# Kernel tuning notes

Measured on AMD Instinct MI355X. Metric: run time of the kernel, lower is better.

Reference implementation:

```python
import jax, jax.numpy as jnp
import numpy as np

B, NP, NL, CIN, COUT, MID = 2048, 8, 4, 256, 256, 64


def setup_inputs() -> dict:
    key = jax.random.key(0)
    ks = jax.random.split(key, 16)
    s = 0.01  # small init scale (code uses xavier_normal with tiny gain)
    inp = {
        "x": jax.random.normal(ks[0], (B, CIN), jnp.float32),
        "h": jax.random.normal(ks[1], (B, NP), jnp.float32),
        "index": jnp.zeros((NL,), jnp.float32).at[0].set(1.0),  # one-hot layer index
        # target Linear params
        "target_w": jax.random.normal(ks[2], (COUT, CIN), jnp.float32) * (1.0 / np.sqrt(CIN)),
        "target_b": jax.random.normal(ks[3], (COUT,), jnp.float32) * 0.01,
        # embedder weight branch
        "fcwp_w": jax.random.normal(ks[4], (MID * CIN, NP), jnp.float32) * s,
        "fcwp_b": jnp.zeros((MID * CIN,), jnp.float32),
        "fcwi_w": jax.random.normal(ks[5], (MID * CIN, NL), jnp.float32) * s,
        "fcwi_b": jnp.zeros((MID * CIN,), jnp.float32),
        "fcwe_w": jax.random.normal(ks[6], (COUT, MID), jnp.float32) * s,
        "fcwe_b": jnp.zeros((COUT,), jnp.float32),
        # embedder bias branch
        "fcbp_w": jax.random.normal(ks[7], (COUT, NP), jnp.float32) * s,
        "fcbp_b": jnp.zeros((COUT,), jnp.float32),
        "fcbi_w": jax.random.normal(ks[8], (COUT, NL), jnp.float32) * s,
        "fcbi_b": jnp.zeros((COUT,), jnp.float32),
    }
    return inp


def reference(x, h, index, target_w, target_b,
              fcwp_w, fcwp_b, fcwi_w, fcwi_b, fcwe_w, fcwe_b,
              fcbp_w, fcbp_b, fcbi_w, fcbi_b):
    # --- embedder: per-sample weight modulation ---
    # w_flat: (B, mid*cin)
    w_flat = h @ fcwp_w.T + fcwp_b + (index @ fcwi_w.T + fcwi_b)
    w = w_flat.reshape(B, CIN, MID)                      # (B, cin, mid)
    w = jnp.einsum('bim,om->boi', w, fcwe_w) + fcwe_b[None, :, None]  # swapaxes folded in -> (B, out, cin)
    # bias modulation: (B, out)
    b = h @ fcbp_w.T + fcbp_b + (index @ fcbi_w.T + fcbi_b)
    # --- per-sample linear (grouped conv2d == batched GEMM) ---
    weights = target_w[None] + w                         # (B, out, cin)
    y = jnp.einsum('bi,boi->bo', x, weights)             # batched matvec
    y = y + target_b[None, :] + b
    return y
```

## Files before the change

### kernel.cpp

```cpp
#include <hip/hip_runtime.h>


#define B_TOT 2048
#define NP    8
#define CIN   256
#define COUT  256
#define MID   64
#define NB1   576
#define K2    352
#define LDG   576
#define LDAS  136
#define LDA2S 360
#define LDB2S 360

typedef short  short8  __attribute__((ext_vector_type(8)));
typedef float  floatx4 __attribute__((ext_vector_type(4)));

__device__ __forceinline__ unsigned short f2bf(float f) {
    union { float f; unsigned u; } v; v.f = f;
    unsigned r = v.u + 0x7FFFu + ((v.u >> 16) & 1u);
    return (unsigned short)(r >> 16);
}
__device__ __forceinline__ float bf2f(unsigned short u) {
    union { unsigned u; float f; } v; v.u = ((unsigned)u) << 16;
    return v.f;
}

__global__ __launch_bounds__(256) void setup_kernel(
    const float* __restrict__ x, const float* __restrict__ h,
    const float* __restrict__ index,
    const float* __restrict__ target_w, const float* __restrict__ target_b,
    const float* __restrict__ fcwp_w, const float* __restrict__ fcwp_b,
    const float* __restrict__ fcwi_w, const float* __restrict__ fcwi_b,
    const float* __restrict__ fcwe_w, const float* __restrict__ fcwe_b,
    const float* __restrict__ fcbp_w, const float* __restrict__ fcbp_b,
    const float* __restrict__ fcbi_w, const float* __restrict__ fcbi_b,
    unsigned short* __restrict__ Bb, unsigned short* __restrict__ B2,
    unsigned short* __restrict__ A2)
{
    __shared__ unsigned short Lt[64][68];
    __shared__ float red[32][8];
    const int blk = blockIdx.x, tid = threadIdx.x;

    if (blk < 32) {
        const int i0 = (blk >> 3) * 64, n0 = (blk & 7) * 64;
        const int r = tid >> 4, c4 = (tid & 15) * 4;
        #pragma unroll
        for (int k = 0; k < 4; ++k) {
            int ii = r + k * 16;
            float4 v = *(const float4*)(fcwp_w + (size_t)(i0 + ii) * 512 + n0 + c4);
            Lt[c4 + 0][ii] = f2bf(v.x); Lt[c4 + 1][ii] = f2bf(v.y);
            Lt[c4 + 2][ii] = f2bf(v.z); Lt[c4 + 3][ii] = f2bf(v.w);
        }
        __syncthreads();
        const int nn = tid >> 2, ic0 = (tid & 3) * 16;
        #pragma unroll
        for (int k = 0; k < 4; ++k) {
            int ic = ic0 + k * 4;
            ushort4 o4;
            o4.x = Lt[nn][ic]; o4.y = Lt[nn][ic + 1];
            o4.z = Lt[nn][ic + 2]; o4.w = Lt[nn][ic + 3];
            *(ushort4*)&Bb[(size_t)(n0 + nn) * CIN + i0 + ic] = o4;
        }
    } else if (blk < 36) {
        const int i0 = (blk - 32) * 64;
        const float x0 = index[0], x1 = index[1], x2 = index[2], x3 = index[3];
        const int r = tid >> 4, c4 = (tid & 15) * 4;
        #pragma unroll
        for (int k = 0; k < 4; ++k) {
            int ii = r + k * 16;
            int e = (i0 + ii) * 64 + c4;
            float4 pb = *(const float4*)(fcwp_b + e);
            float4 ib = *(const float4*)(fcwi_b + e);
            float pbv[4] = {pb.x, pb.y, pb.z, pb.w};
            float ibv[4] = {ib.x, ib.y, ib.z, ib.w};
            #pragma unroll
            for (int j = 0; j < 4; ++j) {
                float4 wv = *(const float4*)(fcwi_w + (size_t)(e + j) * 4);
                Lt[c4 + j][ii] = f2bf(pbv[j] + ibv[j]
                    + x0 * wv.x + x1 * wv.y + x2 * wv.z + x3 * wv.w);
            }
        }
        __syncthreads();
        const int mm = tid >> 2, ic0 = (tid & 3) * 16;
        #pragma unroll
        for (int k = 0; k < 4; ++k) {
            int ic = ic0 + k * 4;
            ushort4 o4;
            o4.x = Lt[mm][ic]; o4.y = Lt[mm][ic + 1];
            o4.z = Lt[mm][ic + 2]; o4.w = Lt[mm][ic + 3];
            *(ushort4*)&Bb[(size_t)(512 + mm) * CIN + i0 + ic] = o4;
        }
    } else if (blk < 52) {
        int base = (blk - 36) * 4096;
        #pragma unroll
        for (int k = 0; k < 4; ++k) {
            int e = base + k * 1024 + tid * 4;
            int o = e >> 8, c = e & 255;
            float4 v = *(const float4*)(target_w + e);
            ushort4 o4;
            o4.x = f2bf(v.x); o4.y = f2bf(v.y); o4.z = f2bf(v.z); o4.w = f2bf(v.w);
            *(ushort4*)&B2[(size_t)o * K2 + c] = o4;
        }
    } else if (blk < 56) {
        int base = (blk - 52) * 4096;
        #pragma unroll
        for (int k = 0; k < 4; ++k) {
            int e = base + k * 1024 + tid * 4;
            int o = e >> 6, m = e & 63;
            float4 v = *(const float4*)(fcwe_w + e);
            ushort4 o4;
            o4.x = f2bf(v.x); o4.y = f2bf(v.y); o4.z = f2bf(v.z); o4.w = f2bf(v.w);
            *(ushort4*)&B2[(size_t)o * K2 + 256 + m] = o4;
        }
    } else if (blk == 56) {
        int o = tid;
        size_t bo = (size_t)o * K2;
        float4 p0 = *(const float4*)(fcbp_w + (size_t)o * 8);
        float4 p1 = *(const float4*)(fcbp_w + (size_t)o * 8 + 4);
        B2[bo + 320] = f2bf(p0.x); B2[bo + 321] = f2bf(p0.y);
        B2[bo + 322] = f2bf(p0.z); B2[bo + 323] = f2bf(p0.w);
        B2[bo + 324] = f2bf(p1.x); B2[bo + 325] = f2bf(p1.y);
        B2[bo + 326] = f2bf(p1.z); B2[bo + 327] = f2bf(p1.w);
        B2[bo + 328] = f2bf(fcwe_b[o]);
        float bc = target_b[o] + fcbp_b[o] + fcbi_b[o]
                 + index[0] * fcbi_w[o * 4]     + index[1] * fcbi_w[o * 4 + 1]
                 + index[2] * fcbi_w[o * 4 + 2] + index[3] * fcbi_w[o * 4 + 3];
        B2[bo + 329] = f2bf(bc);
        #pragma unroll
        for (int z = 330; z < K2; ++z) B2[bo + z] = 0;
    } else {
        const int r0 = (blk - 57) * 32;
        const int rr = tid >> 3, cpos = tid & 7;
        const int b = r0 + rr;
        const float* xrow = x + (size_t)b * CIN;
        float psum = 0.f;
        #pragma unroll
        for (int k = 0; k < 8; ++k) {
            int c = (cpos + k * 8) * 4;
            float4 v = *(const float4*)(xrow + c);
            psum += v.x + v.y + v.z + v.w;
            ushort4 o4;
            o4.x = f2bf(v.x); o4.y = f2bf(v.y); o4.z = f2bf(v.z); o4.w = f2bf(v.w);
            *(ushort4*)&A2[(size_t)b * K2 + c] = o4;
        }
        red[rr][cpos] = psum;
        A2[(size_t)b * K2 + 320 + cpos] = f2bf(h[(size_t)r0 * NP + tid]);
        for (int idx = tid; idx < 32 * 22; idx += 256) {
            int r2 = idx / 22, c2 = 330 + idx % 22;
            A2[(size_t)(r0 + r2) * K2 + c2] = 0;
        }
        __syncthreads();
        if (tid < 32) {
            float s = red[tid][0] + red[tid][1] + red[tid][2] + red[tid][3]
                    + red[tid][4] + red[tid][5] + red[tid][6] + red[tid][7];
            size_t base = (size_t)(r0 + tid) * K2;
            A2[base + 328] = f2bf(s);
            A2[base + 329] = 0x3F80;
        }
    }
}

__global__ __launch_bounds__(256) void gemm1_kernel(
    const unsigned short* __restrict__ A2,
    const unsigned short* __restrict__ Bb,
    unsigned short* __restrict__ G)
{
    __shared__ unsigned short As[64 * LDAS];
    __shared__ unsigned short Bs[64 * LDAS];

    const int tid = threadIdx.x, lane = tid & 63, w = tid >> 6;
    const int col = lane & 15, quad = lane >> 4;
    const int mb = blockIdx.x * 64, nb = blockIdx.y * 64;

    floatx4 acc[4] = {floatx4{0,0,0,0}, floatx4{0,0,0,0},
                      floatx4{0,0,0,0}, floatx4{0,0,0,0}};

    for (int kh = 0; kh < 2; ++kh) {
        const int k0 = kh * 128;
        __syncthreads();
        #pragma unroll
        for (int it = 0; it < 4; ++it) {
            int idx = it * 256 + tid;
            int r = idx >> 4, c = (idx & 15) * 8;
            *(uint4*)&As[r * LDAS + c] =
                *(const uint4*)(A2 + (size_t)(mb + r) * K2 + k0 + c);
            *(uint4*)&Bs[r * LDAS + c] =
                *(const uint4*)(Bb + (size_t)(nb + r) * CIN + k0 + c);
        }
        __syncthreads();
        #pragma unroll
        for (int ks = 0; ks < 4; ++ks) {
            int kc = ks * 32 + quad * 8;
            short8 af = *(const short8*)&As[(w * 16 + col) * LDAS + kc];
            #pragma unroll
            for (int f = 0; f < 4; ++f) {
                short8 bfr = *(const short8*)&Bs[(f * 16 + col) * LDAS + kc];
                acc[f] = __builtin_amdgcn_mfma_f32_16x16x32_bf16(af, bfr, acc[f], 0, 0, 0);
            }
        }
    }
    #pragma unroll
    for (int f = 0; f < 4; ++f)
        #pragma unroll
        for (int r = 0; r < 4; ++r)
            G[(size_t)(mb + w * 16 + quad * 4 + r) * LDG + nb + f * 16 + col]
                = f2bf(acc[f][r]);
}

__global__ __launch_bounds__(256) void gemm2_kernel(
    const unsigned short* __restrict__ A2,
    const unsigned short* __restrict__ B2,
    const unsigned short* __restrict__ G,
    float* __restrict__ out)
{
    __shared__ unsigned short As[32 * LDA2S];
    __shared__ unsigned short Bs[64 * LDB2S];

    const int tid = threadIdx.x, lane = tid & 63, w = tid >> 6;
    const int col = lane & 15, quad = lane >> 4;
    const int b0 = blockIdx.x * 32, n0 = blockIdx.y * 64;

    #pragma unroll
    for (int it = 0; it < 4; ++it) {
        int idx = it * 256 + tid;
        int r = idx >> 5, c = (idx & 31) * 8;
        *(uint4*)&As[r * LDA2S + c] =
            *(const uint4*)(A2 + (size_t)(b0 + r) * K2 + c);
    }
    if (tid < 128) {
        int r = tid >> 2, c = 320 + (tid & 3) * 8;
        *(uint4*)&As[r * LDA2S + c] =
            *(const uint4*)(A2 + (size_t)(b0 + r) * K2 + c);
    }
    #pragma unroll
    for (int it = 0; it < 11; ++it) {
        int idx = it * 256 + tid;
        int r = idx / 44, c = (idx % 44) * 8;
        *(uint4*)&Bs[r * LDB2S + c] =
            *(const uint4*)(B2 + (size_t)(n0 + r) * K2 + c);
    }
    {
        int s = tid >> 3, mg = tid & 7;
        const unsigned short* grow = G + (size_t)(b0 + s) * LDG;
        ushort4 hu0 = *(const ushort4*)(A2 + (size_t)(b0 + s) * K2 + 320);
        ushort4 hu1 = *(const ushort4*)(A2 + (size_t)(b0 + s) * K2 + 324);
        float hv[8] = {bf2f(hu0.x), bf2f(hu0.y), bf2f(hu0.z), bf2f(hu0.w),
                       bf2f(hu1.x), bf2f(hu1.y), bf2f(hu1.z), bf2f(hu1.w)};
        ushort4 cu0 = *(const ushort4*)(grow + 512 + mg * 8);
        ushort4 cu1 = *(const ushort4*)(grow + 512 + mg * 8 + 4);
        float t[8] = {bf2f(cu0.x), bf2f(cu0.y), bf2f(cu0.z), bf2f(cu0.w),
                      bf2f(cu1.x), bf2f(cu1.y), bf2f(cu1.z), bf2f(cu1.w)};
        #pragma unroll
        for (int j = 0; j < 8; ++j) {
            const unsigned short* gp = grow + (mg * 8 + j) * 8;
            ushort4 g0 = *(const ushort4*)gp;
            ushort4 g1 = *(const ushort4*)(gp + 4);
            t[j] += hv[0] * bf2f(g0.x) + hv[1] * bf2f(g0.y)
                  + hv[2] * bf2f(g0.z) + hv[3] * bf2f(g0.w)
                  + hv[4] * bf2f(g1.x) + hv[5] * bf2f(g1.y)
                  + hv[6] * bf2f(g1.z) + hv[7] * bf2f(g1.w);
        }
        ushort4 t0, t1;
        t0.x = f2bf(t[0]); t0.y = f2bf(t[1]); t0.z = f2bf(t[2]); t0.w = f2bf(t[3]);
        t1.x = f2bf(t[4]); t1.y = f2bf(t[5]); t1.z = f2bf(t[6]); t1.w = f2bf(t[7]);
        *(ushort4*)&As[s * LDA2S + 256 + mg * 8]     = t0;
        *(ushort4*)&As[s * LDA2S + 256 + mg * 8 + 4] = t1;
    }
    __syncthreads();

    const int mr = (w & 1) * 16, nbw = (w >> 1) * 32;
    floatx4 acc[2] = {floatx4{0,0,0,0}, floatx4{0,0,0,0}};
    #pragma unroll
    for (int ks = 0; ks < 11; ++ks) {
        int kc = ks * 32 + quad * 8;
        short8 af = *(const short8*)&As[(mr + col) * LDA2S + kc];
        #pragma unroll
        for (int f = 0; f < 2; ++f) {
            short8 bfr = *(const short8*)&Bs[(nbw + f * 16 + col) * LDB2S + kc];
            acc[f] = __builtin_amdgcn_mfma_f32_16x16x32_bf16(af, bfr, acc[f], 0, 0, 0);
        }
    }
    #pragma unroll
    for (int f = 0; f < 2; ++f)
        #pragma unroll
        for (int r = 0; r < 4; ++r)
            out[(size_t)(b0 + mr + quad * 4 + r) * COUT + n0 + nbw + f * 16 + col]
                = acc[f][r];
}

extern "C" void kernel_launch(void* const* d_in, const int* in_sizes, int n_in,
                              void* d_out, int out_size, void* d_ws, size_t ws_size,
                              hipStream_t stream) {
    const float* x        = (const float*)d_in[0];
    const float* h        = (const float*)d_in[1];
    const float* index    = (const float*)d_in[2];
    const float* target_w = (const float*)d_in[3];
    const float* target_b = (const float*)d_in[4];
    const float* fcwp_w   = (const float*)d_in[5];
    const float* fcwp_b   = (const float*)d_in[6];
    const float* fcwi_w   = (const float*)d_in[7];
    const float* fcwi_b   = (const float*)d_in[8];
    const float* fcwe_w   = (const float*)d_in[9];
    const float* fcwe_b   = (const float*)d_in[10];
    const float* fcbp_w   = (const float*)d_in[11];
    const float* fcbp_b   = (const float*)d_in[12];
    const float* fcbi_w   = (const float*)d_in[13];
    const float* fcbi_b   = (const float*)d_in[14];
    float* out = (float*)d_out;

    char* ws = (char*)d_ws;
    unsigned short* Bb = (unsigned short*)ws;
    unsigned short* B2 = (unsigned short*)(ws + 294912);
    unsigned short* A2 = (unsigned short*)(ws + 475136);
    unsigned short* G  = (unsigned short*)(ws + 1916928);

    setup_kernel<<<121, 256, 0, stream>>>(
        x, h, index, target_w, target_b, fcwp_w, fcwp_b, fcwi_w, fcwi_b,
        fcwe_w, fcwe_b, fcbp_w, fcbp_b, fcbi_w, fcbi_b, Bb, B2, A2);

    gemm1_kernel<<<dim3(B_TOT / 64, NB1 / 64), 256, 0, stream>>>(A2, Bb, G);

    gemm2_kernel<<<dim3(B_TOT / 32, COUT / 64), 256, 0, stream>>>(A2, B2, G, out);
}
```

Measured before the change: 93.42 us.

## Fuse setup and both GEMMs into one persistent kernel with grid barriers

Merges the setup kernel and the two GEMM kernels into a single 288-block kernel. The stages are separated by software grid barriers built on per-block flag words in the workspace. The aim is to remove two kernel launches and the gaps between them. In exchange, every block must be co-resident on the device, and each barrier adds spin-wait cost. The flags use fixed magic values and are never reset, so on repeated calls the barriers may pass at once and let stages race.

Measured after the change: 208.1 us. 123% more time.

```diff
diff --git a/kernel.cpp b/kernel.cpp
--- a/kernel.cpp
+++ b/kernel.cpp
@@ -12,6 +12,9 @@
 #define LDAS  136
 #define LDA2S 360
 #define LDB2S 360
+#define GRID  288
+#define MAGIC1 0x13579BDFu
+#define MAGIC2 0x2468ACE1u
 
 typedef short  short8  __attribute__((ext_vector_type(8)));
 typedef float  floatx4 __attribute__((ext_vector_type(4)));
@@ -26,7 +29,25 @@
     return v.f;
 }
 
-__global__ __launch_bounds__(256) void setup_kernel(
+__device__ __forceinline__ void grid_barrier(unsigned* flags, unsigned magic) {
+    __syncthreads();
+    __threadfence();
+    if (threadIdx.x == 0)
+        __hip_atomic_store(&flags[blockIdx.x], magic,
+                           __ATOMIC_RELEASE, __HIP_MEMORY_SCOPE_AGENT);
+    const int t = threadIdx.x;
+    int ok;
+    do {
+        ok = (__hip_atomic_load(&flags[t], __ATOMIC_RELAXED,
+                                __HIP_MEMORY_SCOPE_AGENT) == magic);
+        if (t < GRID - 256)
+            ok = ok && (__hip_atomic_load(&flags[256 + t], __ATOMIC_RELAXED,
+                                          __HIP_MEMORY_SCOPE_AGENT) == magic);
+    } while (!__syncthreads_and(ok));
+    __threadfence();
+}
+
+__global__ __launch_bounds__(256) void hyper_all(
     const float* __restrict__ x, const float* __restrict__ h,
     const float* __restrict__ index,
     const float* __restrict__ target_w, const float* __restrict__ target_b,
@@ -36,257 +57,256 @@
     const float* __restrict__ fcbp_w, const float* __restrict__ fcbp_b,
     const float* __restrict__ fcbi_w, const float* __restrict__ fcbi_b,
     unsigned short* __restrict__ Bb, unsigned short* __restrict__ B2,
-    unsigned short* __restrict__ A2)
+    unsigned short* __restrict__ A2, unsigned short* __restrict__ G,
+    unsigned* __restrict__ flagA, unsigned* __restrict__ flagB,
+    float* __restrict__ out)
 {
-    __shared__ unsigned short Lt[64][68];
-    __shared__ float red[32][8];
+    __shared__ __align__(16) char smem[69120];
     const int blk = blockIdx.x, tid = threadIdx.x;
 
-    if (blk < 32) {
-        const int i0 = (blk >> 3) * 64, n0 = (blk & 7) * 64;
-        const int r = tid >> 4, c4 = (tid & 15) * 4;
-        #pragma unroll
-        for (int k = 0; k < 4; ++k) {
-            int ii = r + k * 16;
-            float4 v = *(const float4*)(fcwp_w + (size_t)(i0 + ii) * 512 + n0 + c4);
-            Lt[c4 + 0][ii] = f2bf(v.x); Lt[c4 + 1][ii] = f2bf(v.y);
-            Lt[c4 + 2][ii] = f2bf(v.z); Lt[c4 + 3][ii] = f2bf(v.w);
-        }
-        __syncthreads();
-        const int nn = tid >> 2, ic0 = (tid & 3) * 16;
-        #pragma unroll
-        for (int k = 0; k < 4; ++k) {
-            int ic = ic0 + k * 4;
-            ushort4 o4;
-            o4.x = Lt[nn][ic]; o4.y = Lt[nn][ic + 1];
-            o4.z = Lt[nn][ic + 2]; o4.w = Lt[nn][ic + 3];
-            *(ushort4*)&Bb[(size_t)(n0 + nn) * CIN + i0 + ic] = o4;
-        }
-    } else if (blk < 36) {
-        const int i0 = (blk - 32) * 64;
-        const float x0 = index[0], x1 = index[1], x2 = index[2], x3 = index[3];
-        const int r = tid >> 4, c4 = (tid & 15) * 4;
-        #pragma unroll
-        for (int k = 0; k < 4; ++k) {
-            int ii = r + k * 16;
-            int e = (i0 + ii) * 64 + c4;
-            float4 pb = *(const float4*)(fcwp_b + e);
-            float4 ib = *(const float4*)(fcwi_b + e);
-            float pbv[4] = {pb.x, pb.y, pb.z, pb.w};
-            float ibv[4] = {ib.x, ib.y, ib.z, ib.w};
-            #pragma unroll
-            for (int j = 0; j < 4; ++j) {
-                float4 wv = *(const float4*)(fcwi_w + (size_t)(e + j) * 4);
-                Lt[c4 + j][ii] = f2bf(pbv[j] + ibv[j]
-                    + x0 * wv.x + x1 * wv.y + x2 * wv.z + x3 * wv.w);
-            }
-        }
-        __syncthreads();
-        const int mm = tid >> 2, ic0 = (tid & 3) * 16;
-        #pragma unroll
-        for (int k = 0; k < 4; ++k) {
-            int ic = ic0 + k * 4;
-            ushort4 o4;
-            o4.x = Lt[mm][ic]; o4.y = Lt[mm][ic + 1];
-            o4.z = Lt[mm][ic + 2]; o4.w = Lt[mm][ic + 3];
-            *(ushort4*)&Bb[(size_t)(512 + mm) * CIN + i0 + ic] = o4;
-        }
-    } else if (blk < 52) {
-        int base = (blk - 36) * 4096;
-        #pragma unroll
-        for (int k = 0; k < 4; ++k) {
-            int e = base + k * 1024 + tid * 4;
-            int o = e >> 8, c = e & 255;
-            float4 v = *(const float4*)(target_w + e);
-            ushort4 o4;
-            o4.x = f2bf(v.x); o4.y = f2bf(v.y); o4.z = f2bf(v.z); o4.w = f2bf(v.w);
-            *(ushort4*)&B2[(size_t)o * K2 + c] = o4;
-        }
-    } else if (blk < 56) {
-        int base = (blk - 52) * 4096;
-        #pragma unroll
-        for (int k = 0; k < 4; ++k) {
-            int e = base + k * 1024 + tid * 4;
-            int o = e >> 6, m = e & 63;
-            float4 v = *(const float4*)(fcwe_w + e);
-            ushort4 o4;
-            o4.x = f2bf(v.x); o4.y = f2bf(v.y); o4.z = f2bf(v.z); o4.w = f2bf(v.w);
-            *(ushort4*)&B2[(size_t)o * K2 + 256 + m] = o4;
-        }
-    } else if (blk == 56) {
-        int o = tid;
-        size_t bo = (size_t)o * K2;
-        float4 p0 = *(const float4*)(fcbp_w + (size_t)o * 8);
-        float4 p1 = *(const float4*)(fcbp_w + (size_t)o * 8 + 4);
-        B2[bo + 320] = f2bf(p0.x); B2[bo + 321] = f2bf(p0.y);
-        B2[bo + 322] = f2bf(p0.z); B2[bo + 323] = f2bf(p0.w);
-        B2[bo + 324] = f2bf(p1.x); B2[bo + 325] = f2bf(p1.y);
-        B2[bo + 326] = f2bf(p1.z); B2[bo + 327] = f2bf(p1.w);
-        B2[bo + 328] = f2bf(fcwe_b[o]);
-        float bc = target_b[o] + fcbp_b[o] + fcbi_b[o]
-                 + index[0] * fcbi_w[o * 4]     + index[1] * fcbi_w[o * 4 + 1]
-                 + index[2] * fcbi_w[o * 4 + 2] + index[3] * fcbi_w[o * 4 + 3];
-        B2[bo + 329] = f2bf(bc);
-        #pragma unroll
-        for (int z = 330; z < K2; ++z) B2[bo + z] = 0;
-    } else {
-        const int r0 = (blk - 57) * 32;
-        const int rr = tid >> 3, cpos = tid & 7;
-        const int b = r0 + rr;
-        const float* xrow = x + (size_t)b * CIN;
-        float psum = 0.f;
-        #pragma unroll
-        for (int k = 0; k < 8; ++k) {
-            int c = (cpos + k * 8) * 4;
-            float4 v = *(const float4*)(xrow + c);
-            psum += v.x + v.y + v.z + v.w;
-            ushort4 o4;
-            o4.x = f2bf(v.x); o4.y = f2bf(v.y); o4.z = f2bf(v.z); o4.w = f2bf(v.w);
-            *(ushort4*)&A2[(size_t)b * K2 + c] = o4;
-        }
-        red[rr][cpos] = psum;
-        A2[(size_t)b * K2 + 320 + cpos] = f2bf(h[(size_t)r0 * NP + tid]);
-        for (int idx = tid; idx < 32 * 22; idx += 256) {
-            int r2 = idx / 22, c2 = 330 + idx % 22;
-            A2[(size_t)(r0 + r2) * K2 + c2] = 0;
-        }
-        __syncthreads();
-        if (tid < 32) {
-            float s = red[tid][0] + red[tid][1] + red[tid][2] + red[tid][3]
-                    + red[tid][4] + red[tid][5] + red[tid][6] + red[tid][7];
-            size_t base = (size_t)(r0 + tid) * K2;
-            A2[base + 328] = f2bf(s);
-            A2[base + 329] = 0x3F80;
+    {
+        unsigned short (*Lt)[68] = (unsigned short (*)[68])smem;
+        float (*red)[8] = (float (*)[8])(smem + 8704);
+
+        if (blk < 32) {
+            const int i0 = (blk >> 3) * 64, n0 = (blk & 7) * 64;
+            const int r = tid >> 4, c4 = (tid & 15) * 4;
+            #pragma unroll
+            for (int k = 0; k < 4; ++k) {
+                int ii = r + k * 16;
+                float4 v = *(const float4*)(fcwp_w + (size_t)(i0 + ii) * 512 + n0 + c4);
+                Lt[c4 + 0][ii] = f2bf(v.x); Lt[c4 + 1][ii] = f2bf(v.y);
+                Lt[c4 + 2][ii] = f2bf(v.z); Lt[c4 + 3][ii] = f2bf(v.w);
+            }
+            __syncthreads();
+            const int nn = tid >> 2, ic0 = (tid & 3) * 16;
+            #pragma unroll
+            for (int k = 0; k < 4; ++k) {
+                int ic = ic0 + k * 4;
+                ushort4 o4;
+                o4.x = Lt[nn][ic]; o4.y = Lt[nn][ic + 1];
+                o4.z = Lt[nn][ic + 2]; o4.w = Lt[nn][ic + 3];
+                *(ushort4*)&Bb[(size_t)(n0 + nn) * CIN + i0 + ic] = o4;
+            }
+        } else if (blk < 36) {
+            const int i0 = (blk - 32) * 64;
+            const float x0 = index[0], x1 = index[1], x2 = index[2], x3 = index[3];
+            const int r = tid >> 4, c4 = (tid & 15) * 4;
+            #pragma unroll
+            for (int k = 0; k < 4; ++k) {
+                int ii = r + k * 16;
+                int e = (i0 + ii) * 64 + c4;
+                float4 pb = *(const float4*)(fcwp_b + e);
+                float4 ib = *(const float4*)(fcwi_b + e);
+                float pbv[4] = {pb.x, pb.y, pb.z, pb.w};
+                float ibv[4] = {ib.x, ib.y, ib.z, ib.w};
+                #pragma unroll
+                for (int j = 0; j < 4; ++j) {
+                    float4 wv = *(const float4*)(fcwi_w + (size_t)(e + j) * 4);
+                    Lt[c4 + j][ii] = f2bf(pbv[j] + ibv[j]
+                        + x0 * wv.x + x1 * wv.y + x2 * wv.z + x3 * wv.w);
+                }
+            }
+            __syncthreads();
+            const int mm = tid >> 2, ic0 = (tid & 3) * 16;
+            #pragma unroll
+            for (int k = 0; k < 4; ++k) {
+                int ic = ic0 + k * 4;
+                ushort4 o4;
+                o4.x = Lt[mm][ic]; o4.y = Lt[mm][ic + 1];
+                o4.z = Lt[mm][ic + 2]; o4.w = Lt[mm][ic + 3];
+                *(ushort4*)&Bb[(size_t)(512 + mm) * CIN + i0 + ic] = o4;
+            }
+        } else if (blk < 52) {
+            int base = (blk - 36) * 4096;
+            #pragma unroll
+            for (int k = 0; k < 4; ++k) {
+                int e = base + k * 1024 + tid * 4;
+                int o = e >> 8, c = e & 255;
+                float4 v = *(const float4*)(target_w + e);
+                ushort4 o4;
+                o4.x = f2bf(v.x); o4.y = f2bf(v.y); o4.z = f2bf(v.z); o4.w = f2bf(v.w);
+                *(ushort4*)&B2[(size_t)o * K2 + c] = o4;
+            }
+        } else if (blk < 56) {
+            int base = (blk - 52) * 4096;
+            #pragma unroll
+            for (int k = 0; k < 4; ++k) {
+                int e = base + k * 1024 + tid * 4;
+                int o = e >> 6, m = e & 63;
+                float4 v = *(const float4*)(fcwe_w + e);
+                ushort4 o4;
+                o4.x = f2bf(v.x); o4.y = f2bf(v.y); o4.z = f2bf(v.z); o4.w = f2bf(v.w);
+                *(ushort4*)&B2[(size_t)o * K2 + 256 + m] = o4;
+            }
+        } else if (blk == 56) {
+            int o = tid;
+            size_t bo = (size_t)o * K2;
+            float4 p0 = *(const float4*)(fcbp_w + (size_t)o * 8);
+            float4 p1 = *(const float4*)(fcbp_w + (size_t)o * 8 + 4);
+            B2[bo + 320] = f2bf(p0.x); B2[bo + 321] = f2bf(p0.y);
+            B2[bo + 322] = f2bf(p0.z); B2[bo + 323] = f2bf(p0.w);
+            B2[bo + 324] = f2bf(p1.x); B2[bo + 325] = f2bf(p1.y);
+            B2[bo + 326] = f2bf(p1.z); B2[bo + 327] = f2bf(p1.w);
+            B2[bo + 328] = f2bf(fcwe_b[o]);
+            float bc = target_b[o] + fcbp_b[o] + fcbi_b[o]
+                     + index[0] * fcbi_w[o * 4]     + index[1] * fcbi_w[o * 4 + 1]
+                     + index[2] * fcbi_w[o * 4 + 2] + index[3] * fcbi_w[o * 4 + 3];
+            B2[bo + 329] = f2bf(bc);
+            #pragma unroll
+            for (int z = 330; z < K2; ++z) B2[bo + z] = 0;
+        } else if (blk < 121) {
+            const int r0 = (blk - 57) * 32;
+            const int rr = tid >> 3, cpos = tid & 7;
+            const int b = r0 + rr;
+            const float* xrow = x + (size_t)b * CIN;
+            float psum = 0.f;
+            #pragma unroll
+            for (int k = 0; k < 8; ++k) {
+                int c = (cpos + k * 8) * 4;
+                float4 v = *(const float4*)(xrow + c);
+                psum += v.x + v.y + v.z + v.w;
+                ushort4 o4;
+                o4.x = f2bf(v.x); o4.y = f2bf(v.y); o4.z = f2bf(v.z); o4.w = f2bf(v.w);
+                *(ushort4*)&A2[(size_t)b * K2 + c] = o4;
+            }
+            red[rr][cpos] = psum;
+            A2[(size_t)b * K2 + 320 + cpos] = f2bf(h[(size_t)r0 * NP + tid]);
+            for (int idx = tid; idx < 32 * 22; idx += 256) {
+                int r2 = idx / 22, c2 = 330 + idx % 22;
+                A2[(size_t)(r0 + r2) * K2 + c2] = 0;
+            }
+            __syncthreads();
+            if (tid < 32) {
+                float s = red[tid][0] + red[tid][1] + red[tid][2] + red[tid][3]
+                        + red[tid][4] + red[tid][5] + red[tid][6] + red[tid][7];
+                size_t base = (size_t)(r0 + tid) * K2;
+                A2[base + 328] = f2bf(s);
+                A2[base + 329] = 0x3F80;
+            }
         }
     }
-}
-
-__global__ __launch_bounds__(256) void gemm1_kernel(
-    const unsigned short* __restrict__ A2,
-    const unsigned short* __restrict__ Bb,
-    unsigned short* __restrict__ G)
-{
-    __shared__ unsigned short As[64 * LDAS];
-    __shared__ unsigned short Bs[64 * LDAS];
-
-    const int tid = threadIdx.x, lane = tid & 63, w = tid >> 6;
-    const int col = lane & 15, quad = lane >> 4;
-    const int mb = blockIdx.x * 64, nb = blockIdx.y * 64;
-
-    floatx4 acc[4] = {floatx4{0,0,0,0}, floatx4{0,0,0,0},
-                      floatx4{0,0,0,0}, floatx4{0,0,0,0}};
-
-    for (int kh = 0; kh < 2; ++kh) {
-        const int k0 = kh * 128;
-        __syncthreads();
+
+    grid_barrier(flagA, MAGIC1);
+
+    {
+        unsigned short* As = (unsigned short*)smem;
+        unsigned short* Bs = (unsigned short*)(smem + 17408);
+        const int lane = tid & 63, w = tid >> 6;
+        const int col = lane & 15, quad = lane >> 4;
+        const int mb = (blk & 31) * 64, nb = (blk >> 5) * 64;
+
+        floatx4 acc[4] = {floatx4{0,0,0,0}, floatx4{0,0,0,0},
+                          floatx4{0,0,0,0}, floatx4{0,0,0,0}};
+
+        for (int kh = 0; kh < 2; ++kh) {
+            const int k0 = kh * 128;
+            __syncthreads();
+            #pragma unroll
+            for (int it = 0; it < 4; ++it) {
+                int idx = it * 256 + tid;
+                int r = idx >> 4, c = (idx & 15) * 8;
+                *(uint4*)&As[r * LDAS + c] =
+                    *(const uint4*)(A2 + (size_t)(mb + r) * K2 + k0 + c);
+                *(uint4*)&Bs[r * LDAS + c] =
+                    *(const uint4*)(Bb + (size_t)(nb + r) * CIN + k0 + c);
+            }
+            __syncthreads();
+            #pragma unroll
+            for (int ks = 0; ks < 4; ++ks) {
+                int kc = ks * 32 + quad * 8;
+                short8 af = *(const short8*)&As[(w * 16 + col) * LDAS + kc];
+                #pragma unroll
+                for (int f = 0; f < 4; ++f) {
+                    short8 bfr = *(const short8*)&Bs[(f * 16 + col) * LDAS + kc];
+                    acc[f] = __builtin_amdgcn_mfma_f32_16x16x32_bf16(af, bfr, acc[f], 0, 0, 0);
+                }
+            }
+        }
+        #pragma unroll
+        for (int f = 0; f < 4; ++f)
+            #pragma unroll
+            for (int r = 0; r < 4; ++r)
+                G[(size_t)(mb + w * 16 + quad * 4 + r) * LDG + nb + f * 16 + col]
+                    = f2bf(acc[f][r]);
+    }
+
+    grid_barrier(flagB, MAGIC2);
+
+    if (blk < 256) {
+        unsigned short* As = (unsigned short*)smem;
+        unsigned short* Bs = (unsigned short*)(smem + 23040);
+        const int lane = tid & 63, w = tid >> 6;
+        const int col = lane & 15, quad = lane >> 4;
+        const int b0 = (blk & 63) * 32, n0 = (blk >> 6) * 64;
+
         #pragma unroll
         for (int it = 0; it < 4; ++it) {
             int idx = it * 256 + tid;
-            int r = idx >> 4, c = (idx & 15) * 8;
-            *(uint4*)&As[r * LDAS + c] =
-                *(const uint4*)(A2 + (size_t)(mb + r) * K2 + k0 + c);
-            *(uint4*)&Bs[r * LDAS + c] =
-                *(const uint4*)(Bb + (size_t)(nb + r) * CIN + k0 + c);
+            int r = idx >> 5, c = (idx & 31) * 8;
+            *(uint4*)&As[r * LDA2S + c] =
+                *(const uint4*)(A2 + (size_t)(b0 + r) * K2 + c);
+        }
+        if (tid < 128) {
+            int r = tid >> 2, c = 320 + (tid & 3) * 8;
+            *(uint4*)&As[r * LDA2S + c] =
+                *(const uint4*)(A2 + (size_t)(b0 + r) * K2 + c);
+        }
+        #pragma unroll
+        for (int it = 0; it < 11; ++it) {
+            int idx = it * 256 + tid;
+            int r = idx / 44, c = (idx % 44) * 8;
+            *(uint4*)&Bs[r * LDB2S + c] =
+                *(const uint4*)(B2 + (size_t)(n0 + r) * K2 + c);
+        }
+        {
+            int s = tid >> 3, mg = tid & 7;
+            const unsigned short* grow = G + (size_t)(b0 + s) * LDG;
+            ushort4 hu0 = *(const ushort4*)(A2 + (size_t)(b0 + s) * K2 + 320);
+            ushort4 hu1 = *(const ushort4*)(A2 + (size_t)(b0 + s) * K2 + 324);
+            float hv[8] = {bf2f(hu0.x), bf2f(hu0.y), bf2f(hu0.z), bf2f(hu0.w),
+                           bf2f(hu1.x), bf2f(hu1.y), bf2f(hu1.z), bf2f(hu1.w)};
+            ushort4 cu0 = *(const ushort4*)(grow + 512 + mg * 8);
+            ushort4 cu1 = *(const ushort4*)(grow + 512 + mg * 8 + 4);
+            float t[8] = {bf2f(cu0.x), bf2f(cu0.y), bf2f(cu0.z), bf2f(cu0.w),
+                          bf2f(cu1.x), bf2f(cu1.y), bf2f(cu1.z), bf2f(cu1.w)};
+            #pragma unroll
+            for (int j = 0; j < 8; ++j) {
+                const unsigned short* gp = grow + (mg * 8 + j) * 8;
+                ushort4 g0 = *(const ushort4*)gp;
+                ushort4 g1 = *(const ushort4*)(gp + 4);
+                t[j] += hv[0] * bf2f(g0.x) + hv[1] * bf2f(g0.y)
+                      + hv[2] * bf2f(g0.z) + hv[3] * bf2f(g0.w)
+                      + hv[4] * bf2f(g1.x) + hv[5] * bf2f(g1.y)
+                      + hv[6] * bf2f(g1.z) + hv[7] * bf2f(g1.w);
+            }
+            ushort4 t0, t1;
+            t0.x = f2bf(t[0]); t0.y = f2bf(t[1]); t0.z = f2bf(t[2]); t0.w = f2bf(t[3]);
+            t1.x = f2bf(t[4]); t1.y = f2bf(t[5]); t1.z = f2bf(t[6]); t1.w = f2bf(t[7]);
+            *(ushort4*)&As[s * LDA2S + 256 + mg * 8]     = t0;
+            *(ushort4*)&As[s * LDA2S + 256 + mg * 8 + 4] = t1;
         }
         __syncthreads();
-        #pragma unroll
-        for (int ks = 0; ks < 4; ++ks) {
+
+        const int mr = (w & 1) * 16, nbw = (w >> 1) * 32;
+        floatx4 acc[2] = {floatx4{0,0,0,0}, floatx4{0,0,0,0}};
+        #pragma unroll
+        for (int ks = 0; ks < 11; ++ks) {
             int kc = ks * 32 + quad * 8;
-            short8 af = *(const short8*)&As[(w * 16 + col) * LDAS + kc];
-            #pragma unroll
-            for (int f = 0; f < 4; ++f) {
-                short8 bfr = *(const short8*)&Bs[(f * 16 + col) * LDAS + kc];
+            short8 af = *(const short8*)&As[(mr + col) * LDA2S + kc];
+            #pragma unroll
+            for (int f = 0; f < 2; ++f) {
+                short8 bfr = *(const short8*)&Bs[(nbw + f * 16 + col) * LDB2S + kc];
                 acc[f] = __builtin_amdgcn_mfma_f32_16x16x32_bf16(af, bfr, acc[f], 0, 0, 0);
             }
         }
+        #pragma unroll
+        for (int f = 0; f < 2; ++f)
+            #pragma unroll
+            for (int r = 0; r < 4; ++r)
+                out[(size_t)(b0 + mr + quad * 4 + r) * COUT + n0 + nbw + f * 16 + col]
+                    = acc[f][r];
     }
-    #pragma unroll
-    for (int f = 0; f < 4; ++f)
-        #pragma unroll
-        for (int r = 0; r < 4; ++r)
-            G[(size_t)(mb + w * 16 + quad * 4 + r) * LDG + nb + f * 16 + col]
-                = f2bf(acc[f][r]);
-}
-
-__global__ __launch_bounds__(256) void gemm2_kernel(
-    const unsigned short* __restrict__ A2,
-    const unsigned short* __restrict__ B2,
-    const unsigned short* __restrict__ G,
-    float* __restrict__ out)
-{
-    __shared__ unsigned short As[32 * LDA2S];
-    __shared__ unsigned short Bs[64 * LDB2S];
-
-    const int tid = threadIdx.x, lane = tid & 63, w = tid >> 6;
-    const int col = lane & 15, quad = lane >> 4;
-    const int b0 = blockIdx.x * 32, n0 = blockIdx.y * 64;
-
-    #pragma unroll
-    for (int it = 0; it < 4; ++it) {
-        int idx = it * 256 + tid;
-        int r = idx >> 5, c = (idx & 31) * 8;
-        *(uint4*)&As[r * LDA2S + c] =
-            *(const uint4*)(A2 + (size_t)(b0 + r) * K2 + c);
-    }
-    if (tid < 128) {
-        int r = tid >> 2, c = 320 + (tid & 3) * 8;
-        *(uint4*)&As[r * LDA2S + c] =
-            *(const uint4*)(A2 + (size_t)(b0 + r) * K2 + c);
-    }
-    #pragma unroll
-    for (int it = 0; it < 11; ++it) {
-        int idx = it * 256 + tid;
-        int r = idx / 44, c = (idx % 44) * 8;
-        *(uint4*)&Bs[r * LDB2S + c] =
-            *(const uint4*)(B2 + (size_t)(n0 + r) * K2 + c);
-    }
-    {
-        int s = tid >> 3, mg = tid & 7;
-        const unsigned short* grow = G + (size_t)(b0 + s) * LDG;
-        ushort4 hu0 = *(const ushort4*)(A2 + (size_t)(b0 + s) * K2 + 320);
-        ushort4 hu1 = *(const ushort4*)(A2 + (size_t)(b0 + s) * K2 + 324);
-        float hv[8] = {bf2f(hu0.x), bf2f(hu0.y), bf2f(hu0.z), bf2f(hu0.w),
-                       bf2f(hu1.x), bf2f(hu1.y), bf2f(hu1.z), bf2f(hu1.w)};
-        ushort4 cu0 = *(const ushort4*)(grow + 512 + mg * 8);
-        ushort4 cu1 = *(const ushort4*)(grow + 512 + mg * 8 + 4);
-        float t[8] = {bf2f(cu0.x), bf2f(cu0.y), bf2f(cu0.z), bf2f(cu0.w),
-                      bf2f(cu1.x), bf2f(cu1.y), bf2f(cu1.z), bf2f(cu1.w)};
-        #pragma unroll
-        for (int j = 0; j < 8; ++j) {
-            const unsigned short* gp = grow + (mg * 8 + j) * 8;
-            ushort4 g0 = *(const ushort4*)gp;
-            ushort4 g1 = *(const ushort4*)(gp + 4);
-            t[j] += hv[0] * bf2f(g0.x) + hv[1] * bf2f(g0.y)
-                  + hv[2] * bf2f(g0.z) + hv[3] * bf2f(g0.w)
-                  + hv[4] * bf2f(g1.x) + hv[5] * bf2f(g1.y)
-                  + hv[6] * bf2f(g1.z) + hv[7] * bf2f(g1.w);
-        }
-        ushort4 t0, t1;
-        t0.x = f2bf(t[0]); t0.y = f2bf(t[1]); t0.z = f2bf(t[2]); t0.w = f2bf(t[3]);
-        t1.x = f2bf(t[4]); t1.y = f2bf(t[5]); t1.z = f2bf(t[6]); t1.w = f2bf(t[7]);
-        *(ushort4*)&As[s * LDA2S + 256 + mg * 8]     = t0;
-        *(ushort4*)&As[s * LDA2S + 256 + mg * 8 + 4] = t1;
-    }
-    __syncthreads();
-
-    const int mr = (w & 1) * 16, nbw = (w >> 1) * 32;
-    floatx4 acc[2] = {floatx4{0,0,0,0}, floatx4{0,0,0,0}};
-    #pragma unroll
-    for (int ks = 0; ks < 11; ++ks) {
-        int kc = ks * 32 + quad * 8;
-        short8 af = *(const short8*)&As[(mr + col) * LDA2S + kc];
-        #pragma unroll
-        for (int f = 0; f < 2; ++f) {
-            short8 bfr = *(const short8*)&Bs[(nbw + f * 16 + col) * LDB2S + kc];
-            acc[f] = __builtin_amdgcn_mfma_f32_16x16x32_bf16(af, bfr, acc[f], 0, 0, 0);
-        }
-    }
-    #pragma unroll
-    for (int f = 0; f < 2; ++f)
-        #pragma unroll
-        for (int r = 0; r < 4; ++r)
-            out[(size_t)(b0 + mr + quad * 4 + r) * COUT + n0 + nbw + f * 16 + col]
-                = acc[f][r];
 }
 
 extern "C" void kernel_launch(void* const* d_in, const int* in_sizes, int n_in,
@@ -314,12 +334,11 @@
     unsigned short* B2 = (unsigned short*)(ws + 294912);
     unsigned short* A2 = (unsigned short*)(ws + 475136);
     unsigned short* G  = (unsigned short*)(ws + 1916928);
-
-    setup_kernel<<<121, 256, 0, stream>>>(
+    unsigned* flagA    = (unsigned*)(ws + 4276224);
+    unsigned* flagB    = (unsigned*)(ws + 4277376);
+
+    hyper_all<<<GRID, 256, 0, stream>>>(
         x, h, index, target_w, target_b, fcwp_w, fcwp_b, fcwi_w, fcwi_b,
-        fcwe_w, fcwe_b, fcbp_w, fcbp_b, fcbi_w, fcbi_b, Bb, B2, A2);
-
-    gemm1_kernel<<<dim3(B_TOT / 64, NB1 / 64), 256, 0, stream>>>(A2, Bb, G);
-
-    gemm2_kernel<<<dim3(B_TOT / 32, COUT / 64), 256, 0, stream>>>(A2, B2, G, out);
-}
+        fcwe_w, fcwe_b, fcbp_w, fcbp_b, fcbi_w, fcbi_b,
+        Bb, B2, A2, G, flagA, flagB, out);
+}
```

## Drop A2 staging buffer; convert x inline in both GEMMs, move B2 prep into gemm1

Applied to the files above, without the earlier changes.

Removes the intermediate bf16 A2 buffer. Both GEMM kernels now read fp32 x and h directly, converting to bf16 in shared memory and computing the row sums of x inside gemm2. The B2 weight-packing blocks move out of the setup kernel and run as extra blocks of gemm1, leaving a smaller setup kernel that only builds Bb. This cuts a global write/read round trip and shortens the setup kernel on the critical path. In exchange gemm1 and gemm2 each read x in fp32, which doubles that traffic, and gemm2 does redundant per-row sums across its column blocks.

After: 94.28 us (median of 2 runs). Within noise of the previous version (+0.9%).

```diff
diff --git a/kernel.cpp b/kernel.cpp
--- a/kernel.cpp
+++ b/kernel.cpp
@@ -6,7 +6,6 @@
 #define CIN   256
 #define COUT  256
 #define MID   64
-#define NB1   576
 #define K2    352
 #define LDG   576
 #define LDAS  136
@@ -26,20 +25,13 @@
     return v.f;
 }
 
-__global__ __launch_bounds__(256) void setup_kernel(
-    const float* __restrict__ x, const float* __restrict__ h,
+__global__ __launch_bounds__(256) void setup_bb(
     const float* __restrict__ index,
-    const float* __restrict__ target_w, const float* __restrict__ target_b,
     const float* __restrict__ fcwp_w, const float* __restrict__ fcwp_b,
     const float* __restrict__ fcwi_w, const float* __restrict__ fcwi_b,
-    const float* __restrict__ fcwe_w, const float* __restrict__ fcwe_b,
-    const float* __restrict__ fcbp_w, const float* __restrict__ fcbp_b,
-    const float* __restrict__ fcbi_w, const float* __restrict__ fcbi_b,
-    unsigned short* __restrict__ Bb, unsigned short* __restrict__ B2,
-    unsigned short* __restrict__ A2)
+    unsigned short* __restrict__ Bb)
 {
     __shared__ unsigned short Lt[64][68];
-    __shared__ float red[32][8];
     const int blk = blockIdx.x, tid = threadIdx.x;
 
     if (blk < 32) {
@@ -62,7 +54,7 @@
             o4.z = Lt[nn][ic + 2]; o4.w = Lt[nn][ic + 3];
             *(ushort4*)&Bb[(size_t)(n0 + nn) * CIN + i0 + ic] = o4;
         }
-    } else if (blk < 36) {
+    } else {
         const int i0 = (blk - 32) * 64;
         const float x0 = index[0], x1 = index[1], x2 = index[2], x3 = index[3];
         const int r = tid >> 4, c4 = (tid & 15) * 4;
@@ -91,8 +83,71 @@
             o4.z = Lt[mm][ic + 2]; o4.w = Lt[mm][ic + 3];
             *(ushort4*)&Bb[(size_t)(512 + mm) * CIN + i0 + ic] = o4;
         }
-    } else if (blk < 52) {
-        int base = (blk - 36) * 4096;
+    }
+}
+
+__global__ __launch_bounds__(256) void gemm1_kernel(
+    const float* __restrict__ x,
+    const unsigned short* __restrict__ Bb,
+    const float* __restrict__ index,
+    const float* __restrict__ target_w, const float* __restrict__ target_b,
+    const float* __restrict__ fcwe_w, const float* __restrict__ fcwe_b,
+    const float* __restrict__ fcbp_w, const float* __restrict__ fcbp_b,
+    const float* __restrict__ fcbi_w, const float* __restrict__ fcbi_b,
+    unsigned short* __restrict__ B2,
+    unsigned short* __restrict__ G)
+{
+    __shared__ unsigned short As[64 * LDAS];
+    __shared__ unsigned short Bs[64 * LDAS];
+    const int blk = blockIdx.x, tid = threadIdx.x;
+
+    if (blk < 288) {
+        const int lane = tid & 63, w = tid >> 6;
+        const int col = lane & 15, quad = lane >> 4;
+        const int mb = (blk & 31) * 64, nb = (blk >> 5) * 64;
+
+        floatx4 acc[4] = {floatx4{0,0,0,0}, floatx4{0,0,0,0},
+                          floatx4{0,0,0,0}, floatx4{0,0,0,0}};
+
+        for (int kh = 0; kh < 2; ++kh) {
+            const int k0 = kh * 128;
+            __syncthreads();
+            #pragma unroll
+            for (int it = 0; it < 8; ++it) {
+                int idx = it * 256 + tid;
+                int r = idx >> 5, c = (idx & 31) * 4;
+                float4 v = *(const float4*)(x + (size_t)(mb + r) * CIN + k0 + c);
+                ushort4 o4;
+                o4.x = f2bf(v.x); o4.y = f2bf(v.y); o4.z = f2bf(v.z); o4.w = f2bf(v.w);
+                *(ushort4*)&As[r * LDAS + c] = o4;
+            }
+            #pragma unroll
+            for (int it = 0; it < 4; ++it) {
+                int idx = it * 256 + tid;
+                int r = idx >> 4, c = (idx & 15) * 8;
+                *(uint4*)&Bs[r * LDAS + c] =
+                    *(const uint4*)(Bb + (size_t)(nb + r) * CIN + k0 + c);
+            }
+            __syncthreads();
+            #pragma unroll
+            for (int ks = 0; ks < 4; ++ks) {
+                int kc = ks * 32 + quad * 8;
+                short8 af = *(const short8*)&As[(w * 16 + col) * LDAS + kc];
+                #pragma unroll
+                for (int f = 0; f < 4; ++f) {
+                    short8 bfr = *(const short8*)&Bs[(f * 16 + col) * LDAS + kc];
+                    acc[f] = __builtin_amdgcn_mfma_f32_16x16x32_bf16(af, bfr, acc[f], 0, 0, 0);
+                }
+            }
+        }
+        #pragma unroll
+        for (int f = 0; f < 4; ++f)
+            #pragma unroll
+            for (int r = 0; r < 4; ++r)
+                G[(size_t)(mb + w * 16 + quad * 4 + r) * LDG + nb + f * 16 + col]
+                    = f2bf(acc[f][r]);
+    } else if (blk < 304) {
+        int base = (blk - 288) * 4096;
         #pragma unroll
         for (int k = 0; k < 4; ++k) {
             int e = base + k * 1024 + tid * 4;
@@ -102,8 +157,8 @@
             o4.x = f2bf(v.x); o4.y = f2bf(v.y); o4.z = f2bf(v.z); o4.w = f2bf(v.w);
             *(ushort4*)&B2[(size_t)o * K2 + c] = o4;
         }
-    } else if (blk < 56) {
-        int base = (blk - 52) * 4096;
+    } else if (blk < 308) {
+        int base = (blk - 304) * 4096;
         #pragma unroll
         for (int k = 0; k < 4; ++k) {
             int e = base + k * 1024 + tid * 4;
@@ -113,7 +168,7 @@
             o4.x = f2bf(v.x); o4.y = f2bf(v.y); o4.z = f2bf(v.z); o4.w = f2bf(v.w);
             *(ushort4*)&B2[(size_t)o * K2 + 256 + m] = o4;
         }
-    } else if (blk == 56) {
+    } else {
         int o = tid;
         size_t bo = (size_t)o * K2;
         float4 p0 = *(const float4*)(fcbp_w + (size_t)o * 8);
@@ -129,109 +184,51 @@
         B2[bo + 329] = f2bf(bc);
         #pragma unroll
         for (int z = 330; z < K2; ++z) B2[bo + z] = 0;
-    } else {
-        const int r0 = (blk - 57) * 32;
-        const int rr = tid >> 3, cpos = tid & 7;
-        const int b = r0 + rr;
-        const float* xrow = x + (size_t)b * CIN;
-        float psum = 0.f;
-        #pragma unroll
-        for (int k = 0; k < 8; ++k) {
-            int c = (cpos + k * 8) * 4;
-            float4 v = *(const float4*)(xrow + c);
-            psum += v.x + v.y + v.z + v.w;
-            ushort4 o4;
-            o4.x = f2bf(v.x); o4.y = f2bf(v.y); o4.z = f2bf(v.z); o4.w = f2bf(v.w);
-            *(ushort4*)&A2[(size_t)b * K2 + c] = o4;
-        }
-        red[rr][cpos] = psum;
-        A2[(size_t)b * K2 + 320 + cpos] = f2bf(h[(size_t)r0 * NP + tid]);
-        for (int idx = tid; idx < 32 * 22; idx += 256) {
-            int r2 = idx / 22, c2 = 330 + idx % 22;
-            A2[(size_t)(r0 + r2) * K2 + c2] = 0;
-        }
-        __syncthreads();
-        if (tid < 32) {
-            float s = red[tid][0] + red[tid][1] + red[tid][2] + red[tid][3]
-                    + red[tid][4] + red[tid][5] + red[tid][6] + red[tid][7];
-            size_t base = (size_t)(r0 + tid) * K2;
-            A2[base + 328] = f2bf(s);
-            A2[base + 329] = 0x3F80;
-        }
-    }
-}
-
-__global__ __launch_bounds__(256) void gemm1_kernel(
-    const unsigned short* __restrict__ A2,
-    const unsigned short* __restrict__ Bb,
-    unsigned short* __restrict__ G)
-{
-    __shared__ unsigned short As[64 * LDAS];
-    __shared__ unsigned short Bs[64 * LDAS];
-
-    const int tid = threadIdx.x, lane = tid & 63, w = tid >> 6;
-    const int col = lane & 15, quad = lane >> 4;
-    const int mb = blockIdx.x * 64, nb = blockIdx.y * 64;
-
-    floatx4 acc[4] = {floatx4{0,0,0,0}, floatx4{0,0,0,0},
-                      floatx4{0,0,0,0}, floatx4{0,0,0,0}};
-
-    for (int kh = 0; kh < 2; ++kh) {
-        const int k0 = kh * 128;
-        __syncthreads();
-        #pragma unroll
-        for (int it = 0; it < 4; ++it) {
-            int idx = it * 256 + tid;
-            int r = idx >> 4, c = (idx & 15) * 8;
-            *(uint4*)&As[r * LDAS + c] =
-                *(const uint4*)(A2 + (size_t)(mb + r) * K2 + k0 + c);
-            *(uint4*)&Bs[r * LDAS + c] =
-                *(const uint4*)(Bb + (size_t)(nb + r) * CIN + k0 + c);
-        }
-        __syncthreads();
-        #pragma unroll
-        for (int ks = 0; ks < 4; ++ks) {
-            int kc = ks * 32 + quad * 8;
-            short8 af = *(const short8*)&As[(w * 16 + col) * LDAS + kc];
-            #pragma unroll
-            for (int f = 0; f < 4; ++f) {
-                short8 bfr = *(const short8*)&Bs[(f * 16 + col) * LDAS + kc];
-                acc[f] = __builtin_amdgcn_mfma_f32_16x16x32_bf16(af, bfr, acc[f], 0, 0, 0);
-            }
-        }
-    }
-    #pragma unroll
-    for (int f = 0; f < 4; ++f)
-        #pragma unroll
-        for (int r = 0; r < 4; ++r)
-            G[(size_t)(mb + w * 16 + quad * 4 + r) * LDG + nb + f * 16 + col]
-                = f2bf(acc[f][r]);
+    }
 }
 
 __global__ __launch_bounds__(256) void gemm2_kernel(
-    const unsigned short* __restrict__ A2,
+    const float* __restrict__ x,
+    const float* __restrict__ h,
     const unsigned short* __restrict__ B2,
     const unsigned short* __restrict__ G,
     float* __restrict__ out)
 {
     __shared__ unsigned short As[32 * LDA2S];
     __shared__ unsigned short Bs[64 * LDB2S];
+    __shared__ float red[32][8];
 
     const int tid = threadIdx.x, lane = tid & 63, w = tid >> 6;
     const int col = lane & 15, quad = lane >> 4;
     const int b0 = blockIdx.x * 32, n0 = blockIdx.y * 64;
 
     #pragma unroll
-    for (int it = 0; it < 4; ++it) {
+    for (int it = 0; it < 8; ++it) {
         int idx = it * 256 + tid;
-        int r = idx >> 5, c = (idx & 31) * 8;
-        *(uint4*)&As[r * LDA2S + c] =
-            *(const uint4*)(A2 + (size_t)(b0 + r) * K2 + c);
-    }
-    if (tid < 128) {
-        int r = tid >> 2, c = 320 + (tid & 3) * 8;
-        *(uint4*)&As[r * LDA2S + c] =
-            *(const uint4*)(A2 + (size_t)(b0 + r) * K2 + c);
+        int r = idx >> 6, c = (idx & 63) * 4;
+        float4 v = *(const float4*)(x + (size_t)(b0 + r) * CIN + c);
+        ushort4 o4;
+        o4.x = f2bf(v.x); o4.y = f2bf(v.y); o4.z = f2bf(v.z); o4.w = f2bf(v.w);
+        *(ushort4*)&As[r * LDA2S + c] = o4;
+    }
+    {
+        int s = tid >> 3, p = tid & 7;
+        As[s * LDA2S + 320 + p] = f2bf(h[(size_t)(b0 + s) * NP + p]);
+    }
+    {
+        int s = tid >> 3, seg = tid & 7;
+        const float* xr = x + (size_t)(b0 + s) * CIN + seg * 32;
+        float p = 0.f;
+        #pragma unroll
+        for (int k = 0; k < 8; ++k) {
+            float4 v = *(const float4*)(xr + k * 4);
+            p += v.x + v.y + v.z + v.w;
+        }
+        red[s][seg] = p;
+    }
+    for (int idx = tid; idx < 32 * 22; idx += 256) {
+        int s = idx / 22, c = 330 + idx % 22;
+        As[s * LDA2S + c] = 0;
     }
     #pragma unroll
     for (int it = 0; it < 11; ++it) {
@@ -243,10 +240,9 @@
     {
         int s = tid >> 3, mg = tid & 7;
         const unsigned short* grow = G + (size_t)(b0 + s) * LDG;
-        ushort4 hu0 = *(const ushort4*)(A2 + (size_t)(b0 + s) * K2 + 320);
-        ushort4 hu1 = *(const ushort4*)(A2 + (size_t)(b0 + s) * K2 + 324);
-        float hv[8] = {bf2f(hu0.x), bf2f(hu0.y), bf2f(hu0.z), bf2f(hu0.w),
-                       bf2f(hu1.x), bf2f(hu1.y), bf2f(hu1.z), bf2f(hu1.w)};
+        float4 h0 = *(const float4*)(h + (size_t)(b0 + s) * NP);
+        float4 h1 = *(const float4*)(h + (size_t)(b0 + s) * NP + 4);
+        float hv[8] = {h0.x, h0.y, h0.z, h0.w, h1.x, h1.y, h1.z, h1.w};
         ushort4 cu0 = *(const ushort4*)(grow + 512 + mg * 8);
         ushort4 cu1 = *(const ushort4*)(grow + 512 + mg * 8 + 4);
         float t[8] = {bf2f(cu0.x), bf2f(cu0.y), bf2f(cu0.z), bf2f(cu0.w),
@@ -266,6 +262,13 @@
         t1.x = f2bf(t[4]); t1.y = f2bf(t[5]); t1.z = f2bf(t[6]); t1.w = f2bf(t[7]);
         *(ushort4*)&As[s * LDA2S + 256 + mg * 8]     = t0;
         *(ushort4*)&As[s * LDA2S + 256 + mg * 8 + 4] = t1;
+    }
+    __syncthreads();
+    if (tid < 32) {
+        float s = red[tid][0] + red[tid][1] + red[tid][2] + red[tid][3]
+                + red[tid][4] + red[tid][5] + red[tid][6] + red[tid][7];
+        As[tid * LDA2S + 328] = f2bf(s);
+        As[tid * LDA2S + 329] = 0x3F80;
     }
     __syncthreads();
 
@@ -312,14 +315,14 @@
     char* ws = (char*)d_ws;
     unsigned short* Bb = (unsigned short*)ws;
     unsigned short* B2 = (unsigned short*)(ws + 294912);
-    unsigned short* A2 = (unsigned short*)(ws + 475136);
-    unsigned short* G  = (unsigned short*)(ws + 1916928);
-
-    setup_kernel<<<121, 256, 0, stream>>>(
-        x, h, index, target_w, target_b, fcwp_w, fcwp_b, fcwi_w, fcwi_b,
-        fcwe_w, fcwe_b, fcbp_w, fcbp_b, fcbi_w, fcbi_b, Bb, B2, A2);
-
-    gemm1_kernel<<<dim3(B_TOT / 64, NB1 / 64), 256, 0, stream>>>(A2, Bb, G);
-
-    gemm2_kernel<<<dim3(B_TOT / 32, COUT / 64), 256, 0, stream>>>(A2, B2, G, out);
-}
+    unsigned short* G  = (unsigned short*)(ws + 475136);
+
+    setup_bb<<<36, 256, 0, stream>>>(index, fcwp_w, fcwp_b, fcwi_w, fcwi_b, Bb);
+
+    gemm1_kernel<<<309, 256, 0, stream>>>(
+        x, Bb, index, target_w, target_b, fcwe_w, fcwe_b,
+        fcbp_w, fcbp_b, fcbi_w, fcbi_b, B2, G);
+
+    gemm2_kernel<<<dim3(B_TOT / 32, COUT / 64), 256, 0, stream>>>(
+        x, h, B2, G, out);
+}
```
